# Performance work log

Hardware: AMD Instinct MI355X
Metric: run time of the kernel (lower is better)

The kernel has to match this reference:

```python
import jax, jax.numpy as jnp
import numpy as np

B = 16384        # batch size
D = 128          # embedding dim == ln_bot[-1]
N_EMB = 26       # number of sparse tables
VOCAB = 50000    # rows per table
LN_BOT = [13, 512, 256, 128]
LN_TOP = [479, 1024, 1024, 512, 1]
# triangular indices matching: li=[i for i in range(ni) for j in range(i)] (offset=0, no self-interaction)
LI, LJ = np.tril_indices(N_EMB + 1, -1)


def _init_linear(key, n_in, n_out):
    kw, kb = jax.random.split(key)
    lim = 1.0 / np.sqrt(n_in)
    W = jax.random.uniform(kw, (n_in, n_out), minval=-lim, maxval=lim, dtype=jnp.float32)
    b = jax.random.uniform(kb, (n_out,), minval=-lim, maxval=lim, dtype=jnp.float32)
    return W, b


def setup_inputs() -> dict:
    key = jax.random.key(0)
    ks = jax.random.split(key, 3 + len(LN_BOT) - 1 + len(LN_TOP) - 1)
    inp = {
        "dense_x": jax.random.normal(ks[0], (B, LN_BOT[0]), dtype=jnp.float32),
        "indices": jax.random.randint(ks[1], (N_EMB, B), 0, VOCAB),
        "emb_tables": jax.random.normal(ks[2], (N_EMB, VOCAB, D), dtype=jnp.float32) * 0.01,
    }
    k = 3
    for i in range(len(LN_BOT) - 1):
        W, b = _init_linear(ks[k], LN_BOT[i], LN_BOT[i + 1]); k += 1
        inp[f"bot_W{i}"], inp[f"bot_b{i}"] = W, b
    for i in range(len(LN_TOP) - 1):
        W, b = _init_linear(ks[k], LN_TOP[i], LN_TOP[i + 1]); k += 1
        inp[f"top_W{i}"], inp[f"top_b{i}"] = W, b
    return inp


def reference(dense_x, indices, emb_tables,
              bot_W0, bot_b0, bot_W1, bot_b1, bot_W2, bot_b2,
              top_W0, top_b0, top_W1, top_b1, top_W2, top_b2, top_W3, top_b3):
    # bottom MLP (sigmoid_bot=-1 -> all ReLU)
    x = dense_x
    for W, b in ((bot_W0, bot_b0), (bot_W1, bot_b1), (bot_W2, bot_b2)):
        x = jax.nn.relu(x @ W + b)                      # [B, 128]

    # embedding lookups (bag size 1 per table)
    emb = jax.vmap(lambda t, i: t[i])(emb_tables, indices)   # [26, B, D]
    emb = jnp.transpose(emb, (1, 0, 2))                      # [B, 26, D]

    # dot interaction
    T = jnp.concatenate([x[:, None, :], emb], axis=1)        # [B, 27, D]
    Z = jnp.einsum('bid,bjd->bij', T, T)                     # [B, 27, 27]
    Zflat = Z[:, LI, LJ]                                     # [B, 351]
    R = jnp.concatenate([x, Zflat], axis=1)                  # [B, 479]

    # top MLP (sigmoid on last layer, sigmoid_top=3)
    h = R
    for W, b in ((top_W0, top_b0), (top_W1, top_b1), (top_W2, top_b2)):
        h = jax.nn.relu(h @ W + b)
    p = jax.nn.sigmoid(h @ top_W3 + top_b3)                  # [B, 1]
    return jnp.clip(p, 0.0, 1.0)                             # loss_threshold = 0.0
```

## Files before the change

### kernel.cpp

```cpp
#include <hip/hip_runtime.h>

typedef __attribute__((ext_vector_type(8))) short short8;
typedef __attribute__((ext_vector_type(4))) float f32x4;
typedef __attribute__((ext_vector_type(16))) float f32x16;

#define B_ROWS 16384

__device__ __forceinline__ float bf2f(ushort u){ return __uint_as_float(((uint)u)<<16); }
__device__ __forceinline__ ushort f2bf(float f){
  uint u = __float_as_uint(f);
  u = u + 0x7FFFu + ((u>>16)&1u);
  return (ushort)(u>>16);
}
__device__ __forceinline__ void gload_lds16(const void* g, void* l){
  __builtin_amdgcn_global_load_lds((const __attribute__((address_space(1))) unsigned*)g,
                                   (__attribute__((address_space(3))) unsigned*)l, 16, 0, 0);
}

struct TArgs { const float* in; ushort* out; int K, N, Kp; };
struct PrepArgs {
  const float* x; const float* W0; const float* b0; ushort* act0;
  TArgs t[5];
  float* partial;
};

__global__ __launch_bounds__(256) void prep(PrepArgs a)
{
  const int idx = blockIdx.x;
  const int tid = threadIdx.x;
  __shared__ float tile[32][33];

  if (idx < 32768){
    int i = idx*256 + tid;
    int b = i>>9, n = i&511;
    const float* xr = a.x + (size_t)b*13;
    float s = a.b0[n];
    #pragma unroll
    for (int k=0;k<13;k++) s += xr[k]*a.W0[k*512+n];
    a.act0[i] = f2bf(fmaxf(s,0.f));
    return;
  }
  if (idx >= 34976){
    a.partial[(idx-34976)*256 + tid] = 0.f;
    return;
  }
  int t = idx - 32768, s, kx, ny;
  if (t < 128)              { s=0; kx=t&15; ny=t>>4; }
  else if ((t-=128) < 32)   { s=1; kx=t&7 ; ny=t>>3; }
  else if ((t-=32) < 512)   { s=2; kx=t&15; ny=t>>4; }
  else if ((t-=512) < 1024) { s=3; kx=t&31; ny=t>>5; }
  else { t-=1024;             s=4; kx=t&31; ny=t>>5; }
  TArgs ta = a.t[s];
  int k0 = kx*32, n0 = ny*32;
  const int c = tid & 31, r8 = tid >> 5;
  #pragma unroll
  for (int p=0;p<4;p++){
    int k = k0 + r8 + p*8;
    tile[r8+p*8][c] = (k < ta.K) ? ta.in[(size_t)k*ta.N + n0 + c] : 0.f;
  }
  __syncthreads();
  #pragma unroll
  for (int p=0;p<4;p++){
    int n = n0 + r8 + p*8;
    ta.out[(size_t)n*ta.Kp + k0 + c] = f2bf(tile[c][r8+p*8]);
  }
}

__global__ __launch_bounds__(256) void bot12(const ushort* __restrict__ act0,
    const ushort* __restrict__ W1t, const float* __restrict__ b1,
    const ushort* __restrict__ W2t, const float* __restrict__ b2,
    ushort* __restrict__ R)
{
  __shared__ __align__(16) char smem[81920];
  const int tid = threadIdx.x;
  const int wave = tid>>6, lane = tid&63;
  const int lr = lane&15, lg = lane>>4;
  const int bm = blockIdx.x*64;

  short8 w2r[2][8];
  #pragma unroll
  for (int n=0;n<2;n++){
    int row = wave*32 + n*16 + lr;
    #pragma unroll
    for (int ks=0;ks<8;ks++)
      w2r[n][ks] = *(const short8*)(W2t + (size_t)row*256 + ks*32 + lg*8);
  }

  auto stage = [&](int buf, int kt){
    #pragma unroll
    for (int c=0;c<2;c++){
      uint lin = (uint)tid*16u + (uint)c*4096u;
      uint row = lin>>7, scol = (lin&127u) ^ (((lin>>7)&7u)<<4);
      gload_lds16((const char*)act0 + (((size_t)(bm+row)*512 + (uint)kt*64u)<<1) + scol,
                  smem + (buf?8192:0) + lin);
    }
    #pragma unroll
    for (int c=0;c<8;c++){
      uint lin = (uint)tid*16u + (uint)c*4096u;
      uint row = lin>>7, scol = (lin&127u) ^ (((lin>>7)&7u)<<4);
      gload_lds16((const char*)W1t + (((size_t)row*512 + (uint)kt*64u)<<1) + scol,
                  smem + 16384 + (buf?32768:0) + lin);
    }
  };

  f32x4 acc[4][4];
  #pragma unroll
  for (int m=0;m<4;m++)
    #pragma unroll
    for (int n=0;n<4;n++)
      #pragma unroll
      for (int j=0;j<4;j++) acc[m][n][j] = 0.f;

  stage(0,0);
  int cur = 0;
  for (int t=0;t<8;t++){
    stage(cur^1, (t+1<8) ? t+1 : 0);
    asm volatile("s_waitcnt vmcnt(10)" ::: "memory");
    __builtin_amdgcn_s_barrier();
    asm volatile("" ::: "memory");
    const char* lAc = smem + (cur?8192:0);
    const char* lBc = smem + 16384 + (cur?32768:0);
    #pragma unroll
    for (int kk2=0;kk2<2;kk2++){
      short8 af[4], bfr[4];
      #pragma unroll
      for (int m=0;m<4;m++){
        uint row = (uint)(m*16+lr);
        uint l = row*128u + (uint)kk2*64u + (uint)lg*16u;
        af[m] = *(const short8*)(lAc + (l ^ ((row&7u)<<4)));
      }
      #pragma unroll
      for (int n=0;n<4;n++){
        uint row = (uint)(wave*64 + n*16+lr);
        uint l = row*128u + (uint)kk2*64u + (uint)lg*16u;
        bfr[n] = *(const short8*)(lBc + (l ^ ((row&7u)<<4)));
      }
      #pragma unroll
      for (int m=0;m<4;m++)
        #pragma unroll
        for (int n=0;n<4;n++)
          acc[m][n] = __builtin_amdgcn_mfma_f32_16x16x32_bf16(af[m], bfr[n], acc[m][n], 0,0,0);
    }
    asm volatile("" ::: "memory");
    __builtin_amdgcn_s_barrier();
    cur ^= 1;
  }
  asm volatile("s_waitcnt vmcnt(0)" ::: "memory");
  __syncthreads();

  ushort* a1 = (ushort*)smem;
  #pragma unroll
  for (int n=0;n<4;n++){
    int col = wave*64 + n*16 + lr;
    float bv = b1[col];
    #pragma unroll
    for (int m=0;m<4;m++)
      #pragma unroll
      for (int j=0;j<4;j++){
        int row = m*16 + lg*4 + j;
        a1[(uint)row*264u + (uint)col] = f2bf(fmaxf(acc[m][n][j] + bv, 0.f));
      }
  }
  __syncthreads();

  f32x4 acc2[4][2];
  #pragma unroll
  for (int m=0;m<4;m++)
    #pragma unroll
    for (int n=0;n<2;n++)
      #pragma unroll
      for (int j=0;j<4;j++) acc2[m][n][j] = 0.f;

  #pragma unroll
  for (int ks=0;ks<8;ks++){
    short8 af[4];
    #pragma unroll
    for (int m=0;m<4;m++)
      af[m] = *(const short8*)&a1[(uint)(m*16+lr)*264u + (uint)ks*32u + (uint)lg*8u];
    #pragma unroll
    for (int m=0;m<4;m++)
      #pragma unroll
      for (int n=0;n<2;n++)
        acc2[m][n] = __builtin_amdgcn_mfma_f32_16x16x32_bf16(af[m], w2r[n][ks], acc2[m][n], 0,0,0);
  }

  #pragma unroll
  for (int n=0;n<2;n++){
    int col = wave*32 + n*16 + lr;
    float bv = b2[col];
    #pragma unroll
    for (int m=0;m<4;m++)
      #pragma unroll
      for (int j=0;j<4;j++){
        int row = bm + m*16 + lg*4 + j;
        R[(size_t)row*512 + col] = f2bf(fmaxf(acc2[m][n][j] + bv, 0.f));
      }
  }
}

template<int BN, bool FUSE>
__global__ __launch_bounds__(512, 2) void gemm256(const ushort* __restrict__ A,
    const ushort* __restrict__ Bt, const float* __restrict__ bias,
    ushort* __restrict__ C, int K, int ldc,
    const float* __restrict__ w3, float* __restrict__ partial)
{
  constexpr int  NF = BN/128;
  constexpr int  LB = BN/128;
  constexpr uint BR = (uint)BN*32u;
  constexpr uint BUFSZ = 16384u + 2u*BR;
  __shared__ __align__(16) ushort lds[2*BUFSZ];

  const int tid = threadIdx.x;
  const int wave = tid>>6, lane = tid&63;
  const uint wm = (uint)(wave>>2), wn = (uint)(wave&3);
  const uint lc = (uint)(lane&31), hi = (uint)(lane>>5);
  const int bm = blockIdx.x*256, bn = blockIdx.y*BN;
  const int nt = K>>6, niter = nt>>1;

  f32x16 acc[4][NF];
  #pragma unroll
  for (int m=0;m<4;m++)
    #pragma unroll
    for (int n=0;n<NF;n++)
      #pragma unroll
      for (int j=0;j<16;j++) acc[m][n][j] = 0.f;

  short8 bfr[2][NF];

#define STAGE(MAT, KH, TILE, SBUF) do{                                          \
    int kt_ = (TILE);                                                           \
    int ktc_ = (kt_ < nt) ? kt_ : 0;                                            \
    const ushort* gb_ = (MAT) ? Bt : A;                                         \
    const uint ro_ = (MAT) ? (uint)bn : (uint)bm;                               \
    const uint rb_ = (uint)(SBUF)*BUFSZ + ((MAT) ? (16384u + (uint)(KH)*BR)     \
                                                 : ((uint)(KH)*8192u));         \
    const int nl_ = (MAT) ? LB : 2;                                             \
    _Pragma("unroll")                                                           \
    for (int j_=0; j_<nl_; ++j_){                                               \
      uint lin_ = (uint)tid*16u + (uint)j_*8192u;                               \
      uint src_ = lin_ ^ (((lin_>>7)&3u)<<4);                                   \
      uint row_ = src_>>6, colb_ = src_&63u;                                    \
      const char* g_ = (const char*)gb_ +                                       \
        (((size_t)(ro_+row_)*(size_t)K + (size_t)ktc_*64 + (KH)*32)<<1) + colb_;\
      gload_lds16(g_, (char*)lds + (size_t)rb_*2 + lin_);                       \
    }                                                                           \
  }while(0)

#define PHASE(CBUF, KKH, MH, BLOAD, SMAT, SKH, STILE, SBUF, CKPT) do{           \
    const uint ab_ = (uint)(CBUF)*BUFSZ + (uint)(KKH)*8192u;                    \
    short8 af_[2][2];                                                           \
    _Pragma("unroll")                                                           \
    for (int mfl_=0; mfl_<2; ++mfl_){                                           \
      uint r_ = wm*128u + ((uint)(MH)*2u+(uint)mfl_)*32u + lc;                  \
      _Pragma("unroll")                                                         \
      for (int k2_=0; k2_<2; ++k2_){                                            \
        uint l_ = r_*64u + hi*16u + (uint)k2_*32u;                              \
        af_[mfl_][k2_] = *(const short8*)((const char*)lds + (size_t)ab_*2      \
                                   + (l_ ^ (((l_>>7)&3u)<<4)));                 \
      }                                                                         \
    }                                                                           \
    if (BLOAD){                                                                 \
      const uint bb_ = (uint)(CBUF)*BUFSZ + 16384u + (uint)(KKH)*BR;            \
      _Pragma("unroll")                                                         \
      for (int nf_=0; nf_<NF; ++nf_){                                           \
        uint r_ = wn*(uint)(BN/4) + (uint)nf_*32u + lc;                         \
        _Pragma("unroll")                                                       \
        for (int k2_=0; k2_<2; ++k2_){                                          \
          uint l_ = r_*64u + hi*16u + (uint)k2_*32u;                            \
          bfr[k2_][nf_] = *(const short8*)((const char*)lds + (size_t)bb_*2     \
                                     + (l_ ^ (((l_>>7)&3u)<<4)));               \
        }                                                                       \
      }                                                                         \
    }                                                                           \
    STAGE(SMAT, SKH, STILE, SBUF);                                              \
    asm volatile("" ::: "memory");                                              \
    __builtin_amdgcn_s_barrier();                                               \
    asm volatile("" ::: "memory");                                              \
    __builtin_amdgcn_s_setprio(1);                                              \
    _Pragma("unroll")                                                           \
    for (int mfl_=0; mfl_<2; ++mfl_)                                            \
      _Pragma("unroll")                                                         \
      for (int nf_=0; nf_<NF; ++nf_)                                            \
        _Pragma("unroll")                                                       \
        for (int k2_=0; k2_<2; ++k2_)                                           \
          acc[(MH)*2+mfl_][nf_] = __builtin_amdgcn_mfma_f32_32x32x16_bf16(      \
              af_[mfl_][k2_], bfr[k2_][nf_], acc[(MH)*2+mfl_][nf_], 0,0,0);     \
    __builtin_amdgcn_s_setprio(0);                                              \
    if (CKPT){                                                                  \
      if constexpr (LB==2) asm volatile("s_waitcnt vmcnt(8)" ::: "memory");     \
      else                 asm volatile("s_waitcnt vmcnt(6)" ::: "memory");     \
    }                                                                           \
    asm volatile("" ::: "memory");                                              \
    __builtin_amdgcn_s_barrier();                                               \
  }while(0)

  STAGE(0,0,0,0); STAGE(1,0,0,0); STAGE(0,1,0,0); STAGE(1,1,0,0);
  STAGE(0,0,1,1); STAGE(1,0,1,1);
  if constexpr (LB==2) asm volatile("s_waitcnt vmcnt(4)" ::: "memory");
  else                 asm volatile("s_waitcnt vmcnt(3)" ::: "memory");
  asm volatile("" ::: "memory");
  __builtin_amdgcn_s_barrier();

  for (int i=0; i<niter; ++i){
    const int O  = 2*i+1;
    const int E2 = 2*i+2;
    const int O2 = 2*i+3;
    PHASE(0,0,0,true , 0,1,O ,1, false);
    PHASE(0,0,1,false, 1,1,O ,1, true );
    PHASE(0,1,0,true , 0,0,E2,0, false);
    PHASE(0,1,1,false, 1,0,E2,0, true );
    PHASE(1,0,0,true , 0,1,E2,0, false);
    PHASE(1,0,1,false, 1,1,E2,0, true );
    PHASE(1,1,0,true , 0,0,O2,1, false);
    PHASE(1,1,1,false, 1,0,O2,1, true );
  }
#undef PHASE
#undef STAGE

  if constexpr (FUSE){
    int col = bn + (int)wn*(BN/4) + (int)lc;
    float bv = bias[col];
    float wv = w3[col];
    #pragma unroll
    for (int mf=0; mf<4; ++mf){
      #pragma unroll
      for (int reg=0; reg<16; ++reg){
        float v = fmaxf(acc[mf][0][reg] + bv, 0.f) * wv;
        #pragma unroll
        for (int off=1; off<32; off<<=1) v += __shfl_xor(v, off);
        if (lc == 0){
          int row = bm + (int)wm*128 + mf*32 + (reg&3) + 8*(reg>>2) + 4*(int)hi;
          atomicAdd(&partial[row], v);
        }
      }
    }
  } else {
    #pragma unroll
    for (int nf=0; nf<NF; ++nf){
      int col = bn + (int)wn*(BN/4) + nf*32 + (int)lc;
      float bv = bias[col];
      #pragma unroll
      for (int mf=0; mf<4; ++mf){
        #pragma unroll
        for (int reg=0; reg<16; ++reg){
          int row = bm + (int)wm*128 + mf*32 + (reg&3) + 8*(reg>>2) + 4*(int)hi;
          float v = acc[mf][nf][reg] + bv;
          C[(size_t)row*ldc + col] = f2bf(fmaxf(v, 0.f));
        }
      }
    }
  }
}

__global__ __launch_bounds__(256) void interact(const int* __restrict__ idx,
    const float* __restrict__ emb, ushort* __restrict__ R)
{
  __shared__ __align__(16) ushort Tl[4][32][136];
  const int w = threadIdx.x>>6, l = threadIdx.x&63;
  const int b = blockIdx.x*4 + w;
  ushort* Rrow = R + (size_t)b*512;

  uint xv = ((const uint*)Rrow)[l];
  *(uint*)&Tl[w][0][2*l] = xv;

  int myidx = (l<26) ? idx[(size_t)l*B_ROWS + b] : 0;
  const int half = l>>5, lc = l&31;
  #pragma unroll
  for (int i=0;i<13;i++){
    const int row = 2*i + 1 + half;
    int e = __shfl(myidx, row - 1);
    const float4* rp = (const float4*)(emb + ((size_t)(row-1)*50000 + (size_t)e)*128);
    float4 v = rp[lc];
    uint2 pk;
    pk.x = (uint)f2bf(v.x) | ((uint)f2bf(v.y)<<16);
    pk.y = (uint)f2bf(v.z) | ((uint)f2bf(v.w)<<16);
    *(uint2*)&Tl[w][row][4*lc] = pk;
  }
  __syncthreads();

  f32x16 acc;
  #pragma unroll
  for (int i=0;i<16;i++) acc[i] = 0.f;
  #pragma unroll
  for (int kk=0;kk<8;kk++){
    short8 fa = *(const short8*)((const char*)&Tl[w][0][0] + (size_t)(l&31)*272 + kk*32 + (l>>5)*16);
    acc = __builtin_amdgcn_mfma_f32_32x32x16_bf16(fa, fa, acc, 0,0,0);
  }

  const int c = l&31;
  #pragma unroll
  for (int j=0;j<16;j++){
    int r = (j&3) + 8*(j>>2) + 4*(l>>5);
    if (c < r && r <= 26) Rrow[128 + r*(r-1)/2 + c] = f2bf(acc[j]);
  }
  if (l < 33) Rrow[479 + l] = 0;
}

__global__ __launch_bounds__(256) void sigm(const float* __restrict__ partial,
    const float* __restrict__ b3, float* __restrict__ out)
{
  int i = blockIdx.x*256 + threadIdx.x;
  float h = partial[i] + b3[0];
  float p = 1.f/(1.f + expf(-h));
  out[i] = fminf(fmaxf(p, 0.f), 1.f);
}

extern "C" void kernel_launch(void* const* d_in, const int* in_sizes, int n_in,
                              void* d_out, int out_size, void* d_ws, size_t ws_size,
                              hipStream_t stream)
{
  const float* dense_x = (const float*)d_in[0];
  const int*   indices = (const int*)d_in[1];
  const float* emb     = (const float*)d_in[2];
  const float* bW0 = (const float*)d_in[3];  const float* bb0 = (const float*)d_in[4];
  const float* bW1 = (const float*)d_in[5];  const float* bb1 = (const float*)d_in[6];
  const float* bW2 = (const float*)d_in[7];  const float* bb2 = (const float*)d_in[8];
  const float* tW0 = (const float*)d_in[9];  const float* tb0 = (const float*)d_in[10];
  const float* tW1 = (const float*)d_in[11]; const float* tb1 = (const float*)d_in[12];
  const float* tW2 = (const float*)d_in[13]; const float* tb2 = (const float*)d_in[14];
  const float* tW3 = (const float*)d_in[15]; const float* tb3 = (const float*)d_in[16];
  float* out = (float*)d_out;
  const int Bn = B_ROWS;

  char* ws = (char*)d_ws;
  size_t o = 0;
  auto alloc = [&](size_t bytes)->char*{ char* r = ws + o; o += (bytes + 255) & ~(size_t)255; return r; };
  ushort* wtB1 = (ushort*)alloc(256*512*2);
  ushort* wtB2 = (ushort*)alloc(128*256*2);
  ushort* wtT0 = (ushort*)alloc(1024*512*2);
  ushort* wtT1 = (ushort*)alloc((size_t)1024*1024*2);
  ushort* wtT2 = (ushort*)alloc(512*1024*2);
  float*  partial = (float*)alloc(B_ROWS*4);
  ushort* P    = (ushort*)alloc((size_t)Bn*512*2);
  ushort* h1   = (ushort*)alloc((size_t)Bn*1024*2);
  ushort* h2   = (ushort*)alloc((size_t)Bn*1024*2);
  (void)ws_size; (void)in_sizes; (void)n_in; (void)out_size;

  PrepArgs pa;
  pa.x = dense_x; pa.W0 = bW0; pa.b0 = bb0; pa.act0 = P;
  pa.t[0] = { bW1, wtB1, 512 , 256 , 512  };
  pa.t[1] = { bW2, wtB2, 256 , 128 , 256  };
  pa.t[2] = { tW0, wtT0, 479 , 1024, 512  };
  pa.t[3] = { tW1, wtT1, 1024, 1024, 1024 };
  pa.t[4] = { tW2, wtT2, 1024, 512 , 1024 };
  pa.partial = partial;
  prep<<<35040,256,0,stream>>>(pa);

  bot12<<<256,256,0,stream>>>(P, wtB1, bb1, wtB2, bb2, P);

  interact<<<Bn/4,256,0,stream>>>(indices, emb, P);

  gemm256<256,false><<<dim3(64,4),512,0,stream>>>(P,  wtT0, tb0, h1, 512 , 1024, nullptr, nullptr);
  gemm256<256,false><<<dim3(64,4),512,0,stream>>>(h1, wtT1, tb1, h2, 1024, 1024, nullptr, nullptr);
  gemm256<128,true ><<<dim3(64,4),512,0,stream>>>(h2, wtT2, tb2, nullptr, 1024, 0, tW3, partial);
  sigm<<<Bn/256,256,0,stream>>>(partial, tb3, out);
}
```

Baseline: 185.4 us.

## Fuse first bottom MLP layer into bot12 kernel, computing act0 in LDS

Moves the 13->512 bottom layer out of the prep kernel and into the bottom-MLP kernel. Each block loads W0 and its 64 input rows into LDS, computes the bf16 activations directly into a swizzled LDS buffer, and the layer-1 MFMA loop reads A fragments from there instead of streaming them from global memory. This removes a 16 MB global write and its re-read, and shrinks the prep launch. In exchange, LDS use per block rises to about 158 KB, which limits each CU to one block, and the layer-0 compute is serialized before the GEMM in only 256 blocks.

```diff
diff --git a/kernel.cpp b/kernel.cpp
--- a/kernel.cpp
+++ b/kernel.cpp
@@ -18,11 +18,7 @@
 }
 
 struct TArgs { const float* in; ushort* out; int K, N, Kp; };
-struct PrepArgs {
-  const float* x; const float* W0; const float* b0; ushort* act0;
-  TArgs t[5];
-  float* partial;
-};
+struct PrepArgs { TArgs t[5]; float* partial; };
 
 __global__ __launch_bounds__(256) void prep(PrepArgs a)
 {
@@ -30,21 +26,11 @@
   const int tid = threadIdx.x;
   __shared__ float tile[32][33];
 
-  if (idx < 32768){
-    int i = idx*256 + tid;
-    int b = i>>9, n = i&511;
-    const float* xr = a.x + (size_t)b*13;
-    float s = a.b0[n];
-    #pragma unroll
-    for (int k=0;k<13;k++) s += xr[k]*a.W0[k*512+n];
-    a.act0[i] = f2bf(fmaxf(s,0.f));
+  if (idx >= 2208){
+    a.partial[(idx-2208)*256 + tid] = 0.f;
     return;
   }
-  if (idx >= 34976){
-    a.partial[(idx-34976)*256 + tid] = 0.f;
-    return;
-  }
-  int t = idx - 32768, s, kx, ny;
+  int t = idx, s, kx, ny;
   if (t < 128)              { s=0; kx=t&15; ny=t>>4; }
   else if ((t-=128) < 32)   { s=1; kx=t&7 ; ny=t>>3; }
   else if ((t-=32) < 512)   { s=2; kx=t&15; ny=t>>4; }
@@ -66,17 +52,27 @@
   }
 }
 
-__global__ __launch_bounds__(256) void bot12(const ushort* __restrict__ act0,
+__global__ __launch_bounds__(256) void bot012(const float* __restrict__ x,
+    const float* __restrict__ W0, const float* __restrict__ b0,
     const ushort* __restrict__ W1t, const float* __restrict__ b1,
     const ushort* __restrict__ W2t, const float* __restrict__ b2,
     ushort* __restrict__ R)
 {
-  __shared__ __align__(16) char smem[81920];
+  __shared__ __align__(16) char smem[161792];
+  float* W0f = (float*)smem;
+  float* xf  = (float*)(smem + 26624);
+  char*  act0 = smem + 30720;
   const int tid = threadIdx.x;
   const int wave = tid>>6, lane = tid&63;
   const int lr = lane&15, lg = lane>>4;
   const int bm = blockIdx.x*64;
 
+  for (int i2=tid; i2<6656; i2+=256) W0f[i2] = W0[i2];
+  for (int i2=tid; i2<1024; i2+=256){
+    int r = i2>>4, c = i2&15;
+    xf[i2] = (c<13) ? x[((size_t)(bm+r))*13 + c] : 0.f;
+  }
+
   short8 w2r[2][8];
   #pragma unroll
   for (int n=0;n<2;n++){
@@ -86,23 +82,45 @@
       w2r[n][ks] = *(const short8*)(W2t + (size_t)row*256 + ks*32 + lg*8);
   }
 
-  auto stage = [&](int buf, int kt){
-    #pragma unroll
-    for (int c=0;c<2;c++){
-      uint lin = (uint)tid*16u + (uint)c*4096u;
-      uint row = lin>>7, scol = (lin&127u) ^ (((lin>>7)&7u)<<4);
-      gload_lds16((const char*)act0 + (((size_t)(bm+row)*512 + (uint)kt*64u)<<1) + scol,
-                  smem + (buf?8192:0) + lin);
-    }
+  auto stageB = [&](int buf, int kt){
     #pragma unroll
     for (int c=0;c<8;c++){
       uint lin = (uint)tid*16u + (uint)c*4096u;
       uint row = lin>>7, scol = (lin&127u) ^ (((lin>>7)&7u)<<4);
       gload_lds16((const char*)W1t + (((size_t)row*512 + (uint)kt*64u)<<1) + scol,
-                  smem + 16384 + (buf?32768:0) + lin);
+                  smem + 96256 + (buf?32768:0) + lin);
     }
   };
 
+  __syncthreads();
+  stageB(0,0);
+
+  {
+    float2 w0c[13];
+    #pragma unroll
+    for (int k=0;k<13;k++) w0c[k] = *(const float2*)&W0f[k*512 + 2*tid];
+    float2 b0v = *(const float2*)&b0[2*tid];
+    #pragma unroll 4
+    for (int r=0;r<64;r++){
+      float4 x0 = *(const float4*)&xf[r*16];
+      float4 x1 = *(const float4*)&xf[r*16+4];
+      float4 x2 = *(const float4*)&xf[r*16+8];
+      float  xc = xf[r*16+12];
+      float sA = b0v.x, sB = b0v.y;
+      sA += x0.x*w0c[0].x + x0.y*w0c[1].x + x0.z*w0c[2].x + x0.w*w0c[3].x;
+      sB += x0.x*w0c[0].y + x0.y*w0c[1].y + x0.z*w0c[2].y + x0.w*w0c[3].y;
+      sA += x1.x*w0c[4].x + x1.y*w0c[5].x + x1.z*w0c[6].x + x1.w*w0c[7].x;
+      sB += x1.x*w0c[4].y + x1.y*w0c[5].y + x1.z*w0c[6].y + x1.w*w0c[7].y;
+      sA += x2.x*w0c[8].x + x2.y*w0c[9].x + x2.z*w0c[10].x + x2.w*w0c[11].x;
+      sB += x2.x*w0c[8].y + x2.y*w0c[9].y + x2.z*w0c[10].y + x2.w*w0c[11].y;
+      sA += xc*w0c[12].x;  sB += xc*w0c[12].y;
+      uint pk = (uint)f2bf(fmaxf(sA,0.f)) | ((uint)f2bf(fmaxf(sB,0.f))<<16);
+      uint a0 = (uint)r*1024u + (uint)tid*4u;
+      *(uint*)(act0 + (a0 ^ (((uint)(r&7))<<4))) = pk;
+    }
+  }
+  __syncthreads();
+
   f32x4 acc[4][4];
   #pragma unroll
   for (int m=0;m<4;m++)
@@ -111,23 +129,20 @@
       #pragma unroll
       for (int j=0;j<4;j++) acc[m][n][j] = 0.f;
 
-  stage(0,0);
   int cur = 0;
   for (int t=0;t<8;t++){
-    stage(cur^1, (t+1<8) ? t+1 : 0);
-    asm volatile("s_waitcnt vmcnt(10)" ::: "memory");
+    stageB(cur^1, (t+1<8) ? t+1 : 0);
+    asm volatile("s_waitcnt vmcnt(8)" ::: "memory");
     __builtin_amdgcn_s_barrier();
     asm volatile("" ::: "memory");
-    const char* lAc = smem + (cur?8192:0);
-    const char* lBc = smem + 16384 + (cur?32768:0);
+    const char* lBc = smem + 96256 + (cur?32768:0);
     #pragma unroll
     for (int kk2=0;kk2<2;kk2++){
       short8 af[4], bfr[4];
       #pragma unroll
       for (int m=0;m<4;m++){
-        uint row = (uint)(m*16+lr);
-        uint l = row*128u + (uint)kk2*64u + (uint)lg*16u;
-        af[m] = *(const short8*)(lAc + (l ^ ((row&7u)<<4)));
+        uint a0 = (uint)(m*16+lr)*1024u + (uint)t*128u + (uint)kk2*64u + (uint)lg*16u;
+        af[m] = *(const short8*)(act0 + (a0 ^ (((uint)(lr&7))<<4)));
       }
       #pragma unroll
       for (int n=0;n<4;n++){
@@ -148,7 +163,7 @@
   asm volatile("s_waitcnt vmcnt(0)" ::: "memory");
   __syncthreads();
 
-  ushort* a1 = (ushort*)smem;
+  ushort* a1 = (ushort*)(smem + 30720);
   #pragma unroll
   for (int n=0;n<4;n++){
     int col = wave*64 + n*16 + lr;
@@ -437,16 +452,15 @@
   (void)ws_size; (void)in_sizes; (void)n_in; (void)out_size;
 
   PrepArgs pa;
-  pa.x = dense_x; pa.W0 = bW0; pa.b0 = bb0; pa.act0 = P;
   pa.t[0] = { bW1, wtB1, 512 , 256 , 512  };
   pa.t[1] = { bW2, wtB2, 256 , 128 , 256  };
   pa.t[2] = { tW0, wtT0, 479 , 1024, 512  };
   pa.t[3] = { tW1, wtT1, 1024, 1024, 1024 };
   pa.t[4] = { tW2, wtT2, 1024, 512 , 1024 };
   pa.partial = partial;
-  prep<<<35040,256,0,stream>>>(pa);
-
-  bot12<<<256,256,0,stream>>>(P, wtB1, bb1, wtB2, bb2, P);
+  prep<<<2272,256,0,stream>>>(pa);
+
+  bot012<<<256,256,0,stream>>>(dense_x, bW0, bb0, wtB1, bb1, wtB2, bb2, P);
 
   interact<<<Bn/4,256,0,stream>>>(indices, emb, P);
 
```

After: 168.3 us, median of 2. 1.1x faster.
